# Kernel tuning notes

Hardware: AMD Instinct MI355X
Metric: run time of the kernel (lower is better)

The kernel has to match this reference:

```python
import jax, jax.numpy as jnp
import numpy as np

N, E, IN_FT, OUT_FT = 8192, 4096, 512, 512
DENSITY = 0.02


def setup_inputs() -> dict:
    key = jax.random.key(0)
    k1, k2, k3, k4 = jax.random.split(key, 4)
    x = jax.random.normal(k1, (N, IN_FT), dtype=jnp.float32)
    hypergraph = (jax.random.uniform(k2, (N, E)) < DENSITY).astype(jnp.float32)
    # kaiming_uniform on [in, out]: fan_in = in_ft (torch fan of a Linear-style 2D param is dim 1 size? torch computes fan_in = size(1) for 2D -> out_ft here)
    bound_w = float(np.sqrt(6.0 / OUT_FT))  # kaiming_uniform a=sqrt(5)? default a=0 -> gain sqrt(2); bound = gain*sqrt(3/fan_in)
    bound_w = float(np.sqrt(2.0) * np.sqrt(3.0 / OUT_FT))
    weight = jax.random.uniform(k3, (IN_FT, OUT_FT), minval=-bound_w, maxval=bound_w, dtype=jnp.float32)
    bound_v = float(np.sqrt(2.0) * np.sqrt(3.0 / 1.0))
    V = jax.random.uniform(k4, (IN_FT, 1), minval=-bound_v, maxval=bound_v, dtype=jnp.float32)
    bias = jnp.zeros((OUT_FT,), dtype=jnp.float32)
    return {"x": x, "hypergraph": hypergraph, "weight": weight, "V": V, "bias": bias}


def reference(x, hypergraph, weight, V, bias):
    # edge embeddings: H^T @ x  -> [E, in_ft]
    edge_emb = hypergraph.T @ x
    hw = jax.nn.sigmoid(edge_emb @ V)          # [E, 1] learned hyperedge weights
    w = hw[:, 0]                                # [E]
    deg_v = (hypergraph @ hw)[:, 0]             # [N]  (sum over last dim of H @ hw)
    deg_e = jnp.sum(hypergraph, axis=0)         # [E]
    # adj = diag(deg_v) @ H @ diag(w) @ diag(deg_e) @ H^T @ diag(deg_v)
    # fused as broadcasted row/col scalings around two GEMMs (same math, no NxN)
    out = x @ weight                            # [N, out_ft]
    t = hypergraph.T @ (deg_v[:, None] * out)   # [E, out_ft]
    t = (w * deg_e)[:, None] * t                # diagonal edge scalings
    out = deg_v[:, None] * (hypergraph @ t)     # [N, out_ft]
    out = out + bias
    return (out, w)
```

## Files before the change

kernel.cpp:

```cpp
#include <hip/hip_runtime.h>


#define N_NODES 8192
#define N_EDGES 4096
#define FT 512

typedef short bf16x8 __attribute__((ext_vector_type(8)));
typedef float f32x4 __attribute__((ext_vector_type(4)));
typedef unsigned short u16;
typedef unsigned int u32;

__device__ __forceinline__ u16 f2b(float f) {
    union { float f; u32 u; } v; v.f = f;
    u32 r = v.u + 0x7FFFu + ((v.u >> 16) & 1u);
    return (u16)(r >> 16);
}
__device__ __forceinline__ float b2f(u16 h) {
    union { u32 u; float f; } v; v.u = ((u32)h) << 16; return v.f;
}


__global__ __launch_bounds__(256) void zero_kernel(float* p, int n) {
    int i = blockIdx.x * 256 + threadIdx.x;
    if (i < n) p[i] = 0.f;
}

__global__ __launch_bounds__(256) void xv_xb_kernel(const float* __restrict__ x,
                                                    const float* __restrict__ V,
                                                    float* __restrict__ xv,
                                                    u16* __restrict__ xb) {
    int row = blockIdx.x * 4 + (threadIdx.x >> 6);
    int lane = threadIdx.x & 63;
    const float* xr = x + (size_t)row * FT + lane * 8;
    const float* vr = V + lane * 8;
    float4 a0 = *(const float4*)xr, a1 = *(const float4*)(xr + 4);
    float4 b0 = *(const float4*)vr, b1 = *(const float4*)(vr + 4);
    float acc = a0.x * b0.x + a0.y * b0.y + a0.z * b0.z + a0.w * b0.w +
                a1.x * b1.x + a1.y * b1.y + a1.z * b1.z + a1.w * b1.w;
    u16 tmp[8] = {f2b(a0.x), f2b(a0.y), f2b(a0.z), f2b(a0.w),
                  f2b(a1.x), f2b(a1.y), f2b(a1.z), f2b(a1.w)};
    *(uint4*)(xb + (size_t)row * FT + lane * 8) = *(uint4*)tmp;
#pragma unroll
    for (int off = 32; off; off >>= 1) acc += __shfl_down(acc, off);
    if (lane == 0) xv[row] = acc;
}

__global__ __launch_bounds__(256) void prep_h4_kernel(const float* __restrict__ H,
                                                      const float* __restrict__ xv,
                                                      u16* __restrict__ Hbf,
                                                      u16* __restrict__ HTbf,
                                                      float* __restrict__ zsum,
                                                      float* __restrict__ desum) {
    __shared__ u32 Wt[64][33];
    __shared__ float xvs[64];
    const int t = threadIdx.x;
    const int e0 = blockIdx.x * 64, n0 = blockIdx.y * 64;
    if (t < 64) xvs[t] = xv[n0 + t];
    const int n_ld = t >> 2, seg = t & 3;
    u32 o[8];
    {
        const float* src = H + (size_t)(n0 + n_ld) * N_EDGES + e0 + seg * 16;
#pragma unroll
        for (int j = 0; j < 4; j++) {
            float4 h = *(const float4*)(src + j * 4);
            o[2 * j]     = (h.x != 0.f ? 0x3F80u : 0u) | (h.y != 0.f ? 0x3F800000u : 0u);
            o[2 * j + 1] = (h.z != 0.f ? 0x3F80u : 0u) | (h.w != 0.f ? 0x3F800000u : 0u);
        }
#pragma unroll
        for (int j = 0; j < 8; j++) Wt[n_ld][seg * 8 + j] = o[j];
    }
    __syncthreads();
    {
        u16* hdst = Hbf + (size_t)(n0 + n_ld) * N_EDGES + e0 + seg * 16;
        *(uint4*)hdst       = *(uint4*)&o[0];
        *(uint4*)(hdst + 8) = *(uint4*)&o[4];
    }
    {
        int e = t >> 2, g = t & 3;
        int ew = e >> 1;
        u32 sel = (e & 1) ? 0x07060302u : 0x05040100u;
        u32 oo[8];
        float z = 0.f, d = 0.f;
#pragma unroll
        for (int j = 0; j < 8; j++) {
            int np = g * 8 + j;
            oo[j] = __builtin_amdgcn_perm(Wt[2 * np + 1][ew], Wt[2 * np][ew], sel);
            z += (oo[j] & 0xFFFFu) ? xvs[2 * np] : 0.f;
            d += (oo[j] & 0xFFFFu) ? 1.f : 0.f;
            z += (oo[j] >> 16) ? xvs[2 * np + 1] : 0.f;
            d += (oo[j] >> 16) ? 1.f : 0.f;
        }
        u32* drow = (u32*)(HTbf + (size_t)(e0 + e) * N_NODES + n0);
        *(uint4*)(drow + g * 8)     = *(uint4*)&oo[0];
        *(uint4*)(drow + g * 8 + 4) = *(uint4*)&oo[4];
        z += __shfl_down(z, 2); z += __shfl_down(z, 1);
        d += __shfl_down(d, 2); d += __shfl_down(d, 1);
        if (g == 0) {
            atomicAdd(zsum + e0 + e, z);
            atomicAdd(desum + e0 + e, d);
        }
    }
}

__global__ __launch_bounds__(256) void sigmoid_kernel(const float* __restrict__ zsum,
                                                      const float* __restrict__ desum,
                                                      float* __restrict__ w_out,
                                                      float* __restrict__ wde) {
    int e = blockIdx.x * 256 + threadIdx.x;
    float z = zsum[e];
    float wv = 1.f / (1.f + expf(-z));
    w_out[e] = wv;
    wde[e] = wv * desum[e];
}

__global__ __launch_bounds__(256) void degv_kernel(const u16* __restrict__ Hbf,
                                                   const float* __restrict__ w,
                                                   float* __restrict__ degv) {
    int row = blockIdx.x * 4 + (threadIdx.x >> 6);
    int lane = threadIdx.x & 63;
    const uint4* hr = (const uint4*)(Hbf + (size_t)row * N_EDGES);
    float acc = 0.f;
#pragma unroll
    for (int i = 0; i < 8; i++) {
        int idx = i * 64 + lane;
        uint4 h = hr[idx];
        const float* w8 = w + idx * 8;
        float4 wa = *(const float4*)w8, wb = *(const float4*)(w8 + 4);
        acc += (h.x & 0xFFFFu) ? wa.x : 0.f;  acc += (h.x >> 16) ? wa.y : 0.f;
        acc += (h.y & 0xFFFFu) ? wa.z : 0.f;  acc += (h.y >> 16) ? wa.w : 0.f;
        acc += (h.z & 0xFFFFu) ? wb.x : 0.f;  acc += (h.z >> 16) ? wb.y : 0.f;
        acc += (h.w & 0xFFFFu) ? wb.z : 0.f;  acc += (h.w >> 16) ? wb.w : 0.f;
    }
#pragma unroll
    for (int off = 32; off; off >>= 1) acc += __shfl_down(acc, off);
    if (lane == 0) degv[row] = acc;
}

__global__ void wt_kernel(const float* __restrict__ src, u16* __restrict__ dst) {
    __shared__ float tile[32][33];
    int tx = threadIdx.x, ty = threadIdx.y;
    int c = blockIdx.x * 32 + tx;
    int r0 = blockIdx.y * 32;
#pragma unroll
    for (int i = 0; i < 4; i++)
        tile[ty + i * 8][tx] = src[(size_t)(r0 + ty + i * 8) * FT + c];
    __syncthreads();
#pragma unroll
    for (int i = 0; i < 4; i++)
        dst[(size_t)(blockIdx.x * 32 + ty + i * 8) * FT + r0 + tx] = f2b(tile[tx][ty + i * 8]);
}

__global__ void t2t_kernel(const u16* __restrict__ P, const float* __restrict__ wde,
                           u16* __restrict__ t2T) {
    __shared__ float tile[32][33];
    int tx = threadIdx.x, ty = threadIdx.y;
    int f0 = blockIdx.x * 32, e0 = blockIdx.y * 32;
#pragma unroll
    for (int i = 0; i < 4; i++) {
        int e = e0 + ty + i * 8;
        size_t idx = (size_t)e * 512 + f0 + tx;
        float s = 0.f;
#pragma unroll
        for (int sl = 0; sl < 8; sl++)
            s += b2f(P[idx + (size_t)sl * N_EDGES * 512]);
        tile[ty + i * 8][tx] = wde[e] * s;
    }
    __syncthreads();
#pragma unroll
    for (int i = 0; i < 4; i++)
        t2T[(size_t)(f0 + ty + i * 8) * N_EDGES + e0 + tx] = f2b(tile[tx][ty + i * 8]);
}

__global__ __launch_bounds__(256) void final_kernel(const u16* __restrict__ P,
                                                    const float* __restrict__ degv,
                                                    const float* __restrict__ bias,
                                                    float* __restrict__ out) {
    int i8 = blockIdx.x * 256 + threadIdx.x;
    int base = i8 * 8;
    int n = base >> 9, f = base & 511;
    float s[8] = {0.f, 0.f, 0.f, 0.f, 0.f, 0.f, 0.f, 0.f};
#pragma unroll
    for (int sl = 0; sl < 4; sl++) {
        uint4 v = *(const uint4*)(P + (size_t)sl * N_NODES * 512 + base);
        u32 ws[4] = {v.x, v.y, v.z, v.w};
#pragma unroll
        for (int j = 0; j < 4; j++) {
            s[2 * j]     += b2f((u16)(ws[j] & 0xFFFFu));
            s[2 * j + 1] += b2f((u16)(ws[j] >> 16));
        }
    }
    float dv = degv[n];
    float4 o0, o1;
    o0.x = dv * s[0] + bias[f + 0]; o0.y = dv * s[1] + bias[f + 1];
    o0.z = dv * s[2] + bias[f + 2]; o0.w = dv * s[3] + bias[f + 3];
    o1.x = dv * s[4] + bias[f + 4]; o1.y = dv * s[5] + bias[f + 5];
    o1.z = dv * s[6] + bias[f + 6]; o1.w = dv * s[7] + bias[f + 7];
    *(float4*)(out + base) = o0;
    *(float4*)(out + base + 4) = o1;
}


#define TBK 64

template <int MT, int NT, int EPI>
__global__ __launch_bounds__(256, 4)
void gemm9(const u16* __restrict__ Ap, const u16* __restrict__ Bp,
           void* __restrict__ Cp, const float* __restrict__ degv,
           int KC, int lda, int ldb, int ldc, size_t Ssz) {
    __shared__ __align__(16) u16 Alds[MT * 32 * TBK];
    __shared__ __align__(16) u16 Blds[NT * 32 * TBK];
    const int t = threadIdx.x;
    const int m0 = blockIdx.x * (MT * 32), n0 = blockIdx.y * (NT * 32);
    const int kbase = blockIdx.z * KC;
    const int wave = t >> 6, lane = t & 63, quad = lane >> 4, lo = lane & 15;
    const int wm = (wave >> 1) * (MT * 16), wn = (wave & 1) * (NT * 16);

    f32x4 acc[MT][NT];
#pragma unroll
    for (int a = 0; a < MT; a++)
#pragma unroll
        for (int b = 0; b < NT; b++) acc[a][b] = (f32x4){0.f, 0.f, 0.f, 0.f};

    for (int kk = 0; kk < KC; kk += TBK) {
        const int k0 = kbase + kk;
        __syncthreads();
#pragma unroll
        for (int i = 0; i < MT; i++) {
            int c = t + i * 256;
            int r = c >> 3;
            int j = ((c & 7) - r) & 7;
            const u16* g = Ap + (size_t)(m0 + r) * lda + k0 + j * 8;
            __builtin_amdgcn_global_load_lds((const u32*)g, (u32*)(Alds + c * 8), 16, 0, 0);
        }
#pragma unroll
        for (int i = 0; i < NT; i++) {
            int c = t + i * 256;
            int r = c >> 3;
            int j = ((c & 7) - r) & 7;
            const u16* g = Bp + (size_t)(n0 + r) * ldb + k0 + j * 8;
            __builtin_amdgcn_global_load_lds((const u32*)g, (u32*)(Blds + c * 8), 16, 0, 0);
        }
        __syncthreads();

#pragma unroll
        for (int s2 = 0; s2 < 2; s2++) {
            bf16x8 af[MT], bfr[NT];
#pragma unroll
            for (int mt = 0; mt < MT; mt++) {
                int m = wm + mt * 16 + lo;
                int s = (s2 * 4 + quad + m) & 7;
                af[mt] = *(const bf16x8*)&Alds[m * TBK + s * 8];
            }
#pragma unroll
            for (int nt = 0; nt < NT; nt++) {
                int n = wn + nt * 16 + lo;
                int s = (s2 * 4 + quad + n) & 7;
                bfr[nt] = *(const bf16x8*)&Blds[n * TBK + s * 8];
            }
#pragma unroll
            for (int mt = 0; mt < MT; mt++)
#pragma unroll
                for (int nt = 0; nt < NT; nt++)
                    acc[mt][nt] = __builtin_amdgcn_mfma_f32_16x16x32_bf16(af[mt], bfr[nt], acc[mt][nt], 0, 0, 0);
        }
    }

    if (EPI == 0) {
        u16* C = (u16*)Cp + (size_t)blockIdx.z * Ssz;
#pragma unroll
        for (int mt = 0; mt < MT; mt++) {
            int rb = m0 + wm + mt * 16 + quad * 4;
#pragma unroll
            for (int i = 0; i < 4; i++)
#pragma unroll
                for (int nt = 0; nt < NT; nt++)
                    C[(size_t)(rb + i) * ldc + n0 + wn + nt * 16 + lo] = f2b(acc[mt][nt][i]);
        }
    } else {
        u16* C = (u16*)Cp;
        float dv[NT];
#pragma unroll
        for (int nt = 0; nt < NT; nt++) dv[nt] = degv[n0 + wn + nt * 16 + lo];
#pragma unroll
        for (int mt = 0; mt < MT; mt++) {
            int rb = m0 + wm + mt * 16 + quad * 4;
#pragma unroll
            for (int i = 0; i < 4; i++)
#pragma unroll
                for (int nt = 0; nt < NT; nt++)
                    C[(size_t)(rb + i) * ldc + n0 + wn + nt * 16 + lo] =
                        f2b(acc[mt][nt][i] * dv[nt]);
        }
    }
}


extern "C" void kernel_launch(void* const* d_in, const int* in_sizes, int n_in,
                              void* d_out, int out_size, void* d_ws, size_t ws_size,
                              hipStream_t stream) {
    const float* x    = (const float*)d_in[0];
    const float* H    = (const float*)d_in[1];
    const float* W    = (const float*)d_in[2];
    const float* V    = (const float*)d_in[3];
    const float* bias = (const float*)d_in[4];
    float* out  = (float*)d_out;
    float* wout = out + (size_t)N_NODES * FT;
    (void)in_sizes; (void)n_in; (void)out_size; (void)ws_size;

    char* wsb = (char*)d_ws;
    float* wsf   = (float*)d_ws;
    float* xv    = wsf;
    float* zsum  = wsf + 8192;
    float* desum = wsf + 12288;
    float* degv  = wsf + 16384;
    float* wde   = wsf + 24576;
    u16*   Hbf   = (u16*)(wsb + 114688);
    u16*   HTbf  = (u16*)(wsb + 67223552);
    u16*   WT    = (u16*)(wsb + 134332416);
    u16*   doutT = (u16*)(wsb + 134856704);
    u16*   t2T   = (u16*)(wsb + 143245312);
    u16*   xb    = (u16*)(wsb + 147439616);
    u16*   P     = (u16*)(wsb + 155828224);

    zero_kernel<<<32, 256, 0, stream>>>(zsum, 8192);
    xv_xb_kernel<<<N_NODES / 4, 256, 0, stream>>>(x, V, xv, xb);
    prep_h4_kernel<<<dim3(N_EDGES / 64, N_NODES / 64), 256, 0, stream>>>(
        H, xv, Hbf, HTbf, zsum, desum);
    sigmoid_kernel<<<N_EDGES / 256, 256, 0, stream>>>(zsum, desum, wout, wde);
    degv_kernel<<<N_NODES / 4, 256, 0, stream>>>(Hbf, wout, degv);
    wt_kernel<<<dim3(16, 16), dim3(32, 8), 0, stream>>>(W, WT);

    gemm9<2, 4, 1><<<dim3(FT / 64, N_NODES / 128, 1), 256, 0, stream>>>(
        WT, xb, doutT, degv, FT, FT, FT, N_NODES, 0);

    gemm9<4, 4, 0><<<dim3(N_EDGES / 128, FT / 128, 8), 256, 0, stream>>>(
        HTbf, doutT, P, nullptr, N_NODES / 8, N_NODES, N_NODES, 512, (size_t)N_EDGES * 512);

    t2t_kernel<<<dim3(FT / 32, N_EDGES / 32), dim3(32, 8), 0, stream>>>(P, wde, t2T);

    gemm9<4, 4, 0><<<dim3(N_NODES / 128, FT / 128, 4), 256, 0, stream>>>(
        Hbf, t2T, P, nullptr, N_EDGES / 4, N_EDGES, N_EDGES, 512, (size_t)N_NODES * 512);

    final_kernel<<<(N_NODES * FT / 8) / 256, 256, 0, stream>>>(P, degv, bias, out);
}
```

Baseline: 354.3 us.

## Store incidence matrix as packed bitmasks and expand to bf16 in GEMM loads

The prep kernel now writes the binary incidence matrix and its transpose as 64-bit bitmasks instead of dense bf16 copies. The degree kernel and both H-based GEMMs read these masks and expand bits into bf16 ones directly in LDS. This cuts the prep-stage writes and the GEMM A-operand traffic from 2 bytes to 1 bit per element. In exchange, the A tile now goes through registers and ordinary LDS stores instead of async global-to-LDS loads, which adds ALU work and may expose more latency.

```diff
diff --git a/kernel.cpp b/kernel.cpp
--- a/kernel.cpp
+++ b/kernel.cpp
@@ -9,6 +9,7 @@
 typedef float f32x4 __attribute__((ext_vector_type(4)));
 typedef unsigned short u16;
 typedef unsigned int u32;
+typedef unsigned long long u64;
 
 __device__ __forceinline__ u16 f2b(float f) {
     union { float f; u32 u; } v; v.f = f;
@@ -45,54 +46,61 @@
     if (lane == 0) xv[row] = acc;
 }
 
-__global__ __launch_bounds__(256) void prep_h4_kernel(const float* __restrict__ H,
-                                                      const float* __restrict__ xv,
-                                                      u16* __restrict__ Hbf,
-                                                      u16* __restrict__ HTbf,
-                                                      float* __restrict__ zsum,
-                                                      float* __restrict__ desum) {
+__global__ __launch_bounds__(256) void prep_b_kernel(const float* __restrict__ H,
+                                                     const float* __restrict__ xv,
+                                                     u64* __restrict__ Hmask,
+                                                     u64* __restrict__ HTmask,
+                                                     float* __restrict__ zsum,
+                                                     float* __restrict__ desum) {
     __shared__ u32 Wt[64][33];
     __shared__ float xvs[64];
     const int t = threadIdx.x;
     const int e0 = blockIdx.x * 64, n0 = blockIdx.y * 64;
     if (t < 64) xvs[t] = xv[n0 + t];
     const int n_ld = t >> 2, seg = t & 3;
-    u32 o[8];
     {
         const float* src = H + (size_t)(n0 + n_ld) * N_EDGES + e0 + seg * 16;
+        u32 m = 0;
+        u32 o[8];
 #pragma unroll
         for (int j = 0; j < 4; j++) {
             float4 h = *(const float4*)(src + j * 4);
             o[2 * j]     = (h.x != 0.f ? 0x3F80u : 0u) | (h.y != 0.f ? 0x3F800000u : 0u);
             o[2 * j + 1] = (h.z != 0.f ? 0x3F80u : 0u) | (h.w != 0.f ? 0x3F800000u : 0u);
+            m |= (h.x != 0.f ? 1u : 0u) << (4 * j);
+            m |= (h.y != 0.f ? 1u : 0u) << (4 * j + 1);
+            m |= (h.z != 0.f ? 1u : 0u) << (4 * j + 2);
+            m |= (h.w != 0.f ? 1u : 0u) << (4 * j + 3);
         }
 #pragma unroll
         for (int j = 0; j < 8; j++) Wt[n_ld][seg * 8 + j] = o[j];
+        u32 mlo = m | (__shfl_down(m, 1) << 16);
+        u32 mhi = __shfl_down(mlo, 2);
+        if (seg == 0)
+            Hmask[(size_t)(n0 + n_ld) * 64 + (e0 >> 6)] = (u64)mlo | ((u64)mhi << 32);
     }
     __syncthreads();
-    {
-        u16* hdst = Hbf + (size_t)(n0 + n_ld) * N_EDGES + e0 + seg * 16;
-        *(uint4*)hdst       = *(uint4*)&o[0];
-        *(uint4*)(hdst + 8) = *(uint4*)&o[4];
-    }
     {
         int e = t >> 2, g = t & 3;
         int ew = e >> 1;
         u32 sel = (e & 1) ? 0x07060302u : 0x05040100u;
-        u32 oo[8];
         float z = 0.f, d = 0.f;
+        u32 m2 = 0;
 #pragma unroll
         for (int j = 0; j < 8; j++) {
             int np = g * 8 + j;
-            oo[j] = __builtin_amdgcn_perm(Wt[2 * np + 1][ew], Wt[2 * np][ew], sel);
-            z += (oo[j] & 0xFFFFu) ? xvs[2 * np] : 0.f;
-            d += (oo[j] & 0xFFFFu) ? 1.f : 0.f;
-            z += (oo[j] >> 16) ? xvs[2 * np + 1] : 0.f;
-            d += (oo[j] >> 16) ? 1.f : 0.f;
-        }
-        u32* drow = (u32*)(HTbf + (size_t)(e0 + e) * N_NODES + n0);
-        *(uint4*)(drow + g * 8)     = *(uint4*)&oo[0];
-        *(uint4*)(drow + g * 8 + 4) = *(uint4*)&oo[4];
+            u32 v = __builtin_amdgcn_perm(Wt[2 * np + 1][ew], Wt[2 * np][ew], sel);
+            z += (v & 0xFFFFu) ? xvs[2 * np] : 0.f;
+            d += (v & 0xFFFFu) ? 1.f : 0.f;
+            z += (v >> 16) ? xvs[2 * np + 1] : 0.f;
+            d += (v >> 16) ? 1.f : 0.f;
+            m2 |= ((v & 0xFFFFu) ? 1u : 0u) << (2 * j);
+            m2 |= ((v >> 16) ? 1u : 0u) << (2 * j + 1);
+        }
+        u32 mlo = m2 | (__shfl_down(m2, 1) << 16);
+        u32 mhi = __shfl_down(mlo, 2);
+        if (g == 0)
+            HTmask[(size_t)(e0 + e) * 128 + (n0 >> 6)] = (u64)mlo | ((u64)mhi << 32);
         z += __shfl_down(z, 2); z += __shfl_down(z, 1);
         d += __shfl_down(d, 2); d += __shfl_down(d, 1);
         if (g == 0) {
@@ -113,23 +121,21 @@
     wde[e] = wv * desum[e];
 }
 
-__global__ __launch_bounds__(256) void degv_kernel(const u16* __restrict__ Hbf,
-                                                   const float* __restrict__ w,
-                                                   float* __restrict__ degv) {
+__global__ __launch_bounds__(256) void degvm_kernel(const u64* __restrict__ Hmask,
+                                                    const float* __restrict__ w,
+                                                    float* __restrict__ degv) {
     int row = blockIdx.x * 4 + (threadIdx.x >> 6);
     int lane = threadIdx.x & 63;
-    const uint4* hr = (const uint4*)(Hbf + (size_t)row * N_EDGES);
+    u64 M = Hmask[(size_t)row * 64 + lane];
+    const float* wl = w + lane * 64;
     float acc = 0.f;
 #pragma unroll
-    for (int i = 0; i < 8; i++) {
-        int idx = i * 64 + lane;
-        uint4 h = hr[idx];
-        const float* w8 = w + idx * 8;
-        float4 wa = *(const float4*)w8, wb = *(const float4*)(w8 + 4);
-        acc += (h.x & 0xFFFFu) ? wa.x : 0.f;  acc += (h.x >> 16) ? wa.y : 0.f;
-        acc += (h.y & 0xFFFFu) ? wa.z : 0.f;  acc += (h.y >> 16) ? wa.w : 0.f;
-        acc += (h.z & 0xFFFFu) ? wb.x : 0.f;  acc += (h.z >> 16) ? wb.y : 0.f;
-        acc += (h.w & 0xFFFFu) ? wb.z : 0.f;  acc += (h.w >> 16) ? wb.w : 0.f;
+    for (int jj = 0; jj < 16; jj++) {
+        float4 wv = *(const float4*)(wl + jj * 4);
+        acc += ((M >> (4 * jj)) & 1ull) ? wv.x : 0.f;
+        acc += ((M >> (4 * jj + 1)) & 1ull) ? wv.y : 0.f;
+        acc += ((M >> (4 * jj + 2)) & 1ull) ? wv.z : 0.f;
+        acc += ((M >> (4 * jj + 3)) & 1ull) ? wv.w : 0.f;
     }
 #pragma unroll
     for (int off = 32; off; off >>= 1) acc += __shfl_down(acc, off);
@@ -202,11 +208,12 @@
 
 #define TBK 64
 
-template <int MT, int NT, int EPI>
+template <int MT, int NT, int EPI, bool AM>
 __global__ __launch_bounds__(256, 4)
-void gemm9(const u16* __restrict__ Ap, const u16* __restrict__ Bp,
-           void* __restrict__ Cp, const float* __restrict__ degv,
-           int KC, int lda, int ldb, int ldc, size_t Ssz) {
+void gemm9(const u16* __restrict__ Ap, const u64* __restrict__ Am,
+           const u16* __restrict__ Bp, void* __restrict__ Cp,
+           const float* __restrict__ degv,
+           int KC, int lda, int ldam, int ldb, int ldc, size_t Ssz) {
     __shared__ __align__(16) u16 Alds[MT * 32 * TBK];
     __shared__ __align__(16) u16 Blds[NT * 32 * TBK];
     const int t = threadIdx.x;
@@ -224,13 +231,30 @@
     for (int kk = 0; kk < KC; kk += TBK) {
         const int k0 = kbase + kk;
         __syncthreads();
-#pragma unroll
-        for (int i = 0; i < MT; i++) {
-            int c = t + i * 256;
-            int r = c >> 3;
-            int j = ((c & 7) - r) & 7;
-            const u16* g = Ap + (size_t)(m0 + r) * lda + k0 + j * 8;
-            __builtin_amdgcn_global_load_lds((const u32*)g, (u32*)(Alds + c * 8), 16, 0, 0);
+        if constexpr (AM) {
+#pragma unroll
+            for (int i = 0; i < MT; i++) {
+                int c = t + i * 256;
+                int r = c >> 3;
+                int j = ((c & 7) - r) & 7;
+                u64 M = Am[(size_t)(m0 + r) * ldam + (k0 >> 6)];
+                u32 b = (u32)(M >> (j * 8)) & 0xFFu;
+                u32 w4[4];
+                w4[0] = (b & 1u   ? 0x3F80u : 0u) | (b & 2u   ? 0x3F800000u : 0u);
+                w4[1] = (b & 4u   ? 0x3F80u : 0u) | (b & 8u   ? 0x3F800000u : 0u);
+                w4[2] = (b & 16u  ? 0x3F80u : 0u) | (b & 32u  ? 0x3F800000u : 0u);
+                w4[3] = (b & 64u  ? 0x3F80u : 0u) | (b & 128u ? 0x3F800000u : 0u);
+                *(uint4*)&Alds[c * 8] = *(uint4*)w4;
+            }
+        } else {
+#pragma unroll
+            for (int i = 0; i < MT; i++) {
+                int c = t + i * 256;
+                int r = c >> 3;
+                int j = ((c & 7) - r) & 7;
+                const u16* g = Ap + (size_t)(m0 + r) * lda + k0 + j * 8;
+                __builtin_amdgcn_global_load_lds((const u32*)g, (u32*)(Alds + c * 8), 16, 0, 0);
+            }
         }
 #pragma unroll
         for (int i = 0; i < NT; i++) {
@@ -314,32 +338,34 @@
     float* desum = wsf + 12288;
     float* degv  = wsf + 16384;
     float* wde   = wsf + 24576;
-    u16*   Hbf   = (u16*)(wsb + 114688);
-    u16*   HTbf  = (u16*)(wsb + 67223552);
-    u16*   WT    = (u16*)(wsb + 134332416);
-    u16*   doutT = (u16*)(wsb + 134856704);
-    u16*   t2T   = (u16*)(wsb + 143245312);
-    u16*   xb    = (u16*)(wsb + 147439616);
-    u16*   P     = (u16*)(wsb + 155828224);
+    u64*   Hmask  = (u64*)(wsb + 114688);
+    u64*   HTmask = (u64*)(wsb + 4308992);
+    u16*   WT     = (u16*)(wsb + 8503296);
+    u16*   doutT  = (u16*)(wsb + 9027584);
+    u16*   t2T    = (u16*)(wsb + 17416192);
+    u16*   xb     = (u16*)(wsb + 21610496);
+    u16*   P      = (u16*)(wsb + 29999104);
 
     zero_kernel<<<32, 256, 0, stream>>>(zsum, 8192);
     xv_xb_kernel<<<N_NODES / 4, 256, 0, stream>>>(x, V, xv, xb);
-    prep_h4_kernel<<<dim3(N_EDGES / 64, N_NODES / 64), 256, 0, stream>>>(
-        H, xv, Hbf, HTbf, zsum, desum);
+    prep_b_kernel<<<dim3(N_EDGES / 64, N_NODES / 64), 256, 0, stream>>>(
+        H, xv, Hmask, HTmask, zsum, desum);
     sigmoid_kernel<<<N_EDGES / 256, 256, 0, stream>>>(zsum, desum, wout, wde);
-    degv_kernel<<<N_NODES / 4, 256, 0, stream>>>(Hbf, wout, degv);
+    degvm_kernel<<<N_NODES / 4, 256, 0, stream>>>(Hmask, wout, degv);
     wt_kernel<<<dim3(16, 16), dim3(32, 8), 0, stream>>>(W, WT);
 
-    gemm9<2, 4, 1><<<dim3(FT / 64, N_NODES / 128, 1), 256, 0, stream>>>(
-        WT, xb, doutT, degv, FT, FT, FT, N_NODES, 0);
-
-    gemm9<4, 4, 0><<<dim3(N_EDGES / 128, FT / 128, 8), 256, 0, stream>>>(
-        HTbf, doutT, P, nullptr, N_NODES / 8, N_NODES, N_NODES, 512, (size_t)N_EDGES * 512);
+    gemm9<2, 4, 1, false><<<dim3(FT / 64, N_NODES / 128, 1), 256, 0, stream>>>(
+        WT, nullptr, xb, doutT, degv, FT, FT, 0, FT, N_NODES, 0);
+
+    gemm9<4, 4, 0, true><<<dim3(N_EDGES / 128, FT / 128, 8), 256, 0, stream>>>(
+        nullptr, HTmask, doutT, P, nullptr, N_NODES / 8, 0, 128, N_NODES, 512,
+        (size_t)N_EDGES * 512);
 
     t2t_kernel<<<dim3(FT / 32, N_EDGES / 32), dim3(32, 8), 0, stream>>>(P, wde, t2T);
 
-    gemm9<4, 4, 0><<<dim3(N_NODES / 128, FT / 128, 4), 256, 0, stream>>>(
-        Hbf, t2T, P, nullptr, N_EDGES / 4, N_EDGES, N_EDGES, 512, (size_t)N_NODES * 512);
+    gemm9<4, 4, 0, true><<<dim3(N_NODES / 128, FT / 128, 4), 256, 0, stream>>>(
+        nullptr, Hmask, t2T, P, nullptr, N_EDGES / 4, 0, 64, N_EDGES, 512,
+        (size_t)N_NODES * 512);
 
     final_kernel<<<(N_NODES * FT / 8) / 256, 256, 0, stream>>>(P, degv, bias, out);
 }
```

Result: no change. 355.2 us (+0.3%).
